# Optimization experiments

Hardware: AMD Instinct MI355X
Metric: run time of the kernel (lower is better)

## Reference

```python
import jax, jax.numpy as jnp
import numpy as np

B, Cin, Cout, H, W = 8, 256, 256, 56, 56
KH, KW, PAD = 3, 3, 1
K = KH * KW
EPS = 1e-5


def _conv3x3(x, w, b):
    # x: [B,Cin,H,W], w: [O,Cin,3,3] -> [B,O,H,W] (stride 1, pad 1)
    y = jax.lax.conv_general_dilated(x, w, window_strides=(1, 1),
                                     padding=((PAD, PAD), (PAD, PAD)),
                                     dimension_numbers=('NCHW', 'OIHW', 'NCHW'))
    return y + b[None, :, None, None]


def _bilinear_gather(x, py, px):
    # x: [B,Cin,H,W]; py/px: [B,K,H,W] fractional sample coords (zero padding)
    y0 = jnp.floor(py); x0 = jnp.floor(px)
    ly = py - y0; lx = px - x0
    y0i = y0.astype(jnp.int32); x0i = x0.astype(jnp.int32)
    y1i = y0i + 1; x1i = x0i + 1
    xf = x.reshape(B, Cin, H * W)

    def corner(yi, xi, wgt):
        valid = ((yi >= 0) & (yi < H) & (xi >= 0) & (xi < W)).astype(x.dtype)
        idx = (jnp.clip(yi, 0, H - 1) * W + jnp.clip(xi, 0, W - 1)).reshape(B, K * H * W)
        v = jax.vmap(lambda xb, ib: xb[:, ib])(xf, idx)  # [B,Cin,K*H*W]
        v = v.reshape(B, Cin, K, H, W)
        return v * (wgt * valid)[:, None]

    return (corner(y0i, x0i, (1 - ly) * (1 - lx)) +
            corner(y0i, x1i, (1 - ly) * lx) +
            corner(y1i, x0i, ly * (1 - lx)) +
            corner(y1i, x1i, ly * lx))


def setup_inputs():
    key = jax.random.key(0)
    ks = jax.random.split(key, 4)
    x = jax.random.normal(ks[0], (B, Cin, H, W), jnp.float32)
    w_off = jax.random.normal(ks[1], (2 * K, Cin, KH, KW), jnp.float32) * 0.01
    b_off = jnp.zeros((2 * K,), jnp.float32)
    w_conv = jax.random.normal(ks[2], (Cout, Cin, KH, KW), jnp.float32) * (1.0 / np.sqrt(Cin * K))
    gamma = jnp.ones((Cout,), jnp.float32)
    beta = jnp.zeros((Cout,), jnp.float32)
    run_mean = jnp.zeros((Cout,), jnp.float32)
    run_var = jnp.ones((Cout,), jnp.float32)
    return {"x": x, "w_off": w_off, "b_off": b_off, "w_conv": w_conv,
            "gamma": gamma, "beta": beta, "run_mean": run_mean, "run_var": run_var}


def reference(x, w_off, b_off, w_conv, gamma, beta, run_mean, run_var):
    # 1) learned offsets: [B, 2K, H, W] -> [B, K, 2(y,x), H, W]
    off = _conv3x3(x, w_off, b_off).reshape(B, K, 2, H, W)
    dy, dx = off[:, :, 0], off[:, :, 1]
    ky = jnp.repeat(jnp.arange(KH, dtype=x.dtype), KW)  # [K]
    kx = jnp.tile(jnp.arange(KW, dtype=x.dtype), KH)
    py = jnp.arange(H, dtype=x.dtype)[None, None, :, None] - PAD + ky[None, :, None, None] + dy
    px = jnp.arange(W, dtype=x.dtype)[None, None, None, :] - PAD + kx[None, :, None, None] + dx
    # 2) bilinear gather -> [B, Cin, K, H, W]; 3) conv reduction over (Cin, K)
    val = _bilinear_gather(x, py, px)
    out = jnp.einsum('bikhw,oik->bohw', val, w_conv.reshape(Cout, Cin, K))
    # 4) BatchNorm (eval: running stats) + ReLU
    inv = gamma / jnp.sqrt(run_var + EPS)
    bn = (out - run_mean[None, :, None, None]) * inv[None, :, None, None] + beta[None, :, None, None]
    return jnp.maximum(bn, 0.0)
```

## Files before the change

### kernel.cpp

```cpp
#include <hip/hip_runtime.h>


#define BATCH 8
#define CIN   256
#define COUT  256
#define HH    56
#define WW    56
#define HW    (HH*WW)
#define NPIX  (BATCH*HW)
#define KTAP  9
#define KG    (KTAP*CIN)
#define NKT   (KG/64)

typedef unsigned short ushortT;
typedef _Float16 f16x8 __attribute__((ext_vector_type(8)));
typedef float f32x4 __attribute__((ext_vector_type(4)));

__device__ __forceinline__ f16x8 lds_ldh8(const ushortT* p) {
    uint4 u = *(const uint4*)p;
    return __builtin_bit_cast(f16x8, u);
}
__device__ __forceinline__ unsigned packh2(float v0, float v1) {
    _Float16 h0 = (_Float16)v0, h1 = (_Float16)v1;
    return (unsigned)__builtin_bit_cast(unsigned short, h0)
         | ((unsigned)__builtin_bit_cast(unsigned short, h1) << 16);
}

__global__ __launch_bounds__(256) void k0_transpose(
    const float* __restrict__ x, float* __restrict__ xt)
{
    __shared__ float t[64][65];
    const int bid = blockIdx.x;
    const int b   = bid / 196;
    const int r   = bid % 196;
    const int hw0 = (r >> 2) * 64;
    const int c0  = (r & 3) * 64;
    const int tid = threadIdx.x;

    {
        const int c_l = tid >> 2, ch = (tid & 3) * 16;
        const float* src = x + ((size_t)(b*CIN + c0 + c_l))*HW + hw0 + ch;
        float4 v0 = *(const float4*)(src + 0);
        float4 v1 = *(const float4*)(src + 4);
        float4 v2 = *(const float4*)(src + 8);
        float4 v3 = *(const float4*)(src + 12);
        *(float4*)&t[c_l][ch + 0]  = v0;
        *(float4*)&t[c_l][ch + 4]  = v1;
        *(float4*)&t[c_l][ch + 8]  = v2;
        *(float4*)&t[c_l][ch + 12] = v3;
    }
    __syncthreads();
    {
        const int hw_l = tid >> 2, cc = (tid & 3) * 16;
        float* dst = xt + ((size_t)(b*HW + hw0 + hw_l))*CIN + c0 + cc;
        #pragma unroll
        for (int q = 0; q < 4; ++q) {
            float4 o;
            o.x = t[cc + q*4 + 0][hw_l];
            o.y = t[cc + q*4 + 1][hw_l];
            o.z = t[cc + q*4 + 2][hw_l];
            o.w = t[cc + q*4 + 3][hw_l];
            *(float4*)(dst + q*4) = o;
        }
    }
}

__global__ void k2a_prep_w(const float* __restrict__ wconv, const float* __restrict__ woff,
                           ushortT* __restrict__ Ah, ushortT* __restrict__ A0h)
{
    int id = blockIdx.x*256 + threadIdx.x;
    if (id < COUT*KG) {
        int m = id / KG, kg = id % KG;
        int k = kg >> 8, i = kg & 255;
        float f = wconv[(m*CIN + i)*9 + k];
        int kt = kg >> 6, kk = kg & 63;
        _Float16 h = (_Float16)f;
        Ah[kt*16384 + m*64 + (kk ^ ((m & 7) << 3))] = __builtin_bit_cast(unsigned short, h);
    } else if (id < COUT*KG + 32*KG) {
        int id2 = id - COUT*KG;
        int m = id2 / KG, kg = id2 % KG;
        int k = kg >> 8, i = kg & 255;
        float f = (m < 18) ? woff[(m*CIN + i)*9 + k] : 0.f;
        int kt = kg >> 6, kk = kg & 63;
        _Float16 h = (_Float16)f;
        A0h[kt*2048 + m*64 + (kk ^ ((m & 7) << 3))] = __builtin_bit_cast(unsigned short, h);
    }
}

__global__ __launch_bounds__(256) void k1_offmfma(
    const float* __restrict__ xt, const ushortT* __restrict__ A0h_g,
    const float* __restrict__ b_off, float* __restrict__ off)
{
    __shared__ __align__(16) ushortT A0[32*64];
    __shared__ __align__(16) ushortT Bh[64*64];

    const int tid = threadIdx.x;
    const int bn0 = blockIdx.x * 64;
    const int wv = tid >> 6, lane = tid & 63;
    const int l16 = lane & 15, lq = lane >> 4;
    const int px_l = tid >> 2, g2 = tid & 3;

    const int np = bn0 + px_l;
    const int hw = np % HW;
    const int h = hw / WW, w = hw % WW;

    f32x4 acc[2] = {};

    for (int kt = 0; kt < NKT; ++kt) {
        const int tap = kt >> 2, ic = kt & 3;
        const int ky = tap / 3 - 1, kx = tap % 3 - 1;
        __syncthreads();
        __builtin_amdgcn_global_load_lds(
            (const __attribute__((address_space(1))) unsigned*)((const char*)A0h_g + kt*4096 + tid*16),
            (__attribute__((address_space(3))) unsigned*)((char*)A0 + wv*1024), 16, 0, 0);
        {
            const int hs = h + ky, ws = w + kx;
            const bool valid = (hs >= 0 && hs < HH && ws >= 0 && ws < WW);
            const float* p = xt + ((size_t)(np + ky*WW + kx))*CIN + ic*64 + g2*16;
            float4 v0, v1, v2, v3;
            if (valid) {
                v0 = *(const float4*)(p + 0);  v1 = *(const float4*)(p + 4);
                v2 = *(const float4*)(p + 8);  v3 = *(const float4*)(p + 12);
            } else {
                v0 = v1 = v2 = v3 = make_float4(0.f, 0.f, 0.f, 0.f);
            }
            uint4 h0, h1;
            h0.x = packh2(v0.x, v0.y); h0.y = packh2(v0.z, v0.w);
            h0.z = packh2(v1.x, v1.y); h0.w = packh2(v1.z, v1.w);
            h1.x = packh2(v2.x, v2.y); h1.y = packh2(v2.z, v2.w);
            h1.z = packh2(v3.x, v3.y); h1.w = packh2(v3.z, v3.w);
            const int base = g2 * 16;
            *(uint4*)&Bh[px_l*64 + ((base + 0) ^ ((px_l & 7) << 3))] = h0;
            *(uint4*)&Bh[px_l*64 + ((base + 8) ^ ((px_l & 7) << 3))] = h1;
        }
        __syncthreads();
        #pragma unroll
        for (int ks = 0; ks < 2; ++ks) {
            const int kk0 = ks*32 + lq*8;
            f16x8 a0, a1, b;
            {
                const int m0 = l16, m1 = 16 + l16;
                a0 = lds_ldh8(&A0[m0*64 + (kk0 ^ ((m0 & 7) << 3))]);
                a1 = lds_ldh8(&A0[m1*64 + (kk0 ^ ((m1 & 7) << 3))]);
            }
            {
                const int n = wv*16 + l16;
                b = lds_ldh8(&Bh[n*64 + (kk0 ^ ((n & 7) << 3))]);
            }
            acc[0] = __builtin_amdgcn_mfma_f32_16x16x32_f16(a0, b, acc[0], 0, 0, 0);
            acc[1] = __builtin_amdgcn_mfma_f32_16x16x32_f16(a1, b, acc[1], 0, 0, 0);
        }
    }
    const int n = bn0 + wv*16 + l16;
    const int b2 = n / HW, hw2 = n % HW;
    #pragma unroll
    for (int mf = 0; mf < 2; ++mf) {
        #pragma unroll
        for (int r = 0; r < 4; ++r) {
            const int m = mf*16 + lq*4 + r;
            if (m < 18)
                off[((size_t)b2*18 + m)*HW + hw2] = acc[mf][r] + b_off[m];
        }
    }
}

__global__ void k2b_meta(const float* __restrict__ off,
                         int* __restrict__ midx, float* __restrict__ mw)
{
    int id = blockIdx.x*256 + threadIdx.x;
    if (id >= KTAP*NPIX) return;
    int k = id / NPIX, np = id % NPIX;
    int b = np / HW, hw = np % HW;
    int h = hw / WW, w = hw % WW;
    float dy = off[((size_t)b*18 + 2*k    )*HW + hw];
    float dx = off[((size_t)b*18 + 2*k + 1)*HW + hw];
    float py = (float)(h - 1 + (k / 3)) + dy;
    float px = (float)(w - 1 + (k % 3)) + dx;
    py = fminf(fmaxf(py, -10000.f), 10000.f);
    px = fminf(fmaxf(px, -10000.f), 10000.f);
    float y0f = floorf(py), x0f = floorf(px);
    int y0 = (int)y0f, x0 = (int)x0f;
    float ly = py - y0f, lx = px - x0f;
    #pragma unroll
    for (int c = 0; c < 4; ++c) {
        int yi = y0 + (c >> 1), xi = x0 + (c & 1);
        float wgt = ((c >> 1) ? ly : 1.f - ly) * ((c & 1) ? lx : 1.f - lx);
        bool valid = (yi >= 0 && yi < HH && xi >= 0 && xi < WW);
        int yc = min(max(yi, 0), HH-1), xc = min(max(xi, 0), WW-1);
        midx[(c*KTAP + k)*NPIX + np] = (b*HW + yc*WW + xc) * CIN;
        mw  [(c*KTAP + k)*NPIX + np] = valid ? wgt : 0.f;
    }
}

__global__ void k2c_bn(const float* __restrict__ g, const float* __restrict__ be,
                       const float* __restrict__ rm, const float* __restrict__ rv,
                       float* __restrict__ scale, float* __restrict__ shift)
{
    int t = threadIdx.x;
    float inv = g[t] / sqrtf(rv[t] + 1e-5f);
    scale[t] = inv;
    shift[t] = be[t] - rm[t]*inv;
}

__global__ __launch_bounds__(512) void k3_main(
    const float* __restrict__ xt, const int* __restrict__ midx, const float* __restrict__ mw,
    const ushortT* __restrict__ Ah_g, const float* __restrict__ scale_g,
    const float* __restrict__ shift_g, float* __restrict__ out)
{
    __shared__ __align__(16) ushortT Ah_t[256*64];
    __shared__ __align__(16) ushortT Bh_t[64*64];
    __shared__ __align__(16) ushortT Bl_t[64*64];
    __shared__ int   s_midx[256];
    __shared__ float s_mw[256];
    __shared__ float s_scale[256], s_shift[256];

    const int tid = threadIdx.x;
    const int bn0 = blockIdx.x * 64;
    if (tid < 256) { s_scale[tid] = scale_g[tid]; s_shift[tid] = shift_g[tid]; }

    const int wv = tid >> 6, lane = tid & 63;
    const int l16 = lane & 15, lq = lane >> 4;
    const int mbase = (wv >> 1) * 64;
    const int nbase = (wv & 1) * 32;
    const int px_l = tid >> 3, g = tid & 7;

    f32x4 acc[4][2] = {};

    for (int kt = 0; kt < NKT; ++kt) {
        const int tap = kt >> 2, ic = kt & 3;
        __syncthreads();
        if (ic == 0) {
            if (tid < 256) {
                const int c = tid >> 6, px = tid & 63;
                s_midx[tid] = midx[(c*KTAP + tap)*NPIX + bn0 + px];
                s_mw[tid]   = mw  [(c*KTAP + tap)*NPIX + bn0 + px];
            }
            __syncthreads();
        }
        {
            const char* gh = (const char*)Ah_g + (size_t)kt*32768;
            #pragma unroll
            for (int it = 0; it < 4; ++it) {
                __builtin_amdgcn_global_load_lds(
                    (const __attribute__((address_space(1))) unsigned*)(gh + it*8192 + tid*16),
                    (__attribute__((address_space(3))) unsigned*)((char*)Ah_t + it*8192 + wv*1024), 16, 0, 0);
            }
        }
        {
            const float* base = xt + (size_t)(ic*64 + g*8);
            const float* p0 = base + s_midx[0*64 + px_l]; const float fw0 = s_mw[0*64 + px_l];
            const float* p1 = base + s_midx[1*64 + px_l]; const float fw1 = s_mw[1*64 + px_l];
            const float* p2 = base + s_midx[2*64 + px_l]; const float fw2 = s_mw[2*64 + px_l];
            const float* p3 = base + s_midx[3*64 + px_l]; const float fw3 = s_mw[3*64 + px_l];
            float4 a0 = *(const float4*)(p0 + 0), a1 = *(const float4*)(p0 + 4);
            float4 b0 = *(const float4*)(p1 + 0), b1 = *(const float4*)(p1 + 4);
            float4 c0 = *(const float4*)(p2 + 0), c1 = *(const float4*)(p2 + 4);
            float4 d0 = *(const float4*)(p3 + 0), d1 = *(const float4*)(p3 + 4);
            float v[8];
            v[0] = fw0*a0.x + fw1*b0.x + fw2*c0.x + fw3*d0.x;
            v[1] = fw0*a0.y + fw1*b0.y + fw2*c0.y + fw3*d0.y;
            v[2] = fw0*a0.z + fw1*b0.z + fw2*c0.z + fw3*d0.z;
            v[3] = fw0*a0.w + fw1*b0.w + fw2*c0.w + fw3*d0.w;
            v[4] = fw0*a1.x + fw1*b1.x + fw2*c1.x + fw3*d1.x;
            v[5] = fw0*a1.y + fw1*b1.y + fw2*c1.y + fw3*d1.y;
            v[6] = fw0*a1.z + fw1*b1.z + fw2*c1.z + fw3*d1.z;
            v[7] = fw0*a1.w + fw1*b1.w + fw2*c1.w + fw3*d1.w;
            uint4 hi, lo;
            float r[8];
            #pragma unroll
            for (int j = 0; j < 8; ++j) {
                _Float16 hh = (_Float16)v[j];
                r[j] = v[j] - (float)hh;
            }
            hi.x = packh2(v[0], v[1]); hi.y = packh2(v[2], v[3]);
            hi.z = packh2(v[4], v[5]); hi.w = packh2(v[6], v[7]);
            lo.x = packh2(r[0], r[1]); lo.y = packh2(r[2], r[3]);
            lo.z = packh2(r[4], r[5]); lo.w = packh2(r[6], r[7]);
            const int idx = px_l*64 + ((g*8) ^ ((px_l & 7) << 3));
            *(uint4*)&Bh_t[idx] = hi;
            *(uint4*)&Bl_t[idx] = lo;
        }
        __syncthreads();
        #pragma unroll
        for (int ks = 0; ks < 2; ++ks) {
            const int kk0 = ks*32 + lq*8;
            f16x8 a[4], bh[2], bl[2];
            #pragma unroll
            for (int mf = 0; mf < 4; ++mf) {
                const int m = mbase + mf*16 + l16;
                a[mf] = lds_ldh8(&Ah_t[m*64 + (kk0 ^ ((m & 7) << 3))]);
            }
            #pragma unroll
            for (int nf = 0; nf < 2; ++nf) {
                const int n = nbase + nf*16 + l16;
                const int idx = n*64 + (kk0 ^ ((n & 7) << 3));
                bh[nf] = lds_ldh8(&Bh_t[idx]);
                bl[nf] = lds_ldh8(&Bl_t[idx]);
            }
            #pragma unroll
            for (int mf = 0; mf < 4; ++mf) {
                #pragma unroll
                for (int nf = 0; nf < 2; ++nf) {
                    acc[mf][nf] = __builtin_amdgcn_mfma_f32_16x16x32_f16(a[mf], bh[nf], acc[mf][nf], 0, 0, 0);
                    acc[mf][nf] = __builtin_amdgcn_mfma_f32_16x16x32_f16(a[mf], bl[nf], acc[mf][nf], 0, 0, 0);
                }
            }
        }
    }
    #pragma unroll
    for (int mf = 0; mf < 4; ++mf) {
        #pragma unroll
        for (int nf = 0; nf < 2; ++nf) {
            const int n = bn0 + nbase + nf*16 + l16;
            const int b = n / HW, hw = n % HW;
            const int m0 = mbase + mf*16 + lq*4;
            float* op = out + ((size_t)b*COUT + m0)*HW + hw;
            const f32x4 v = acc[mf][nf];
            #pragma unroll
            for (int r = 0; r < 4; ++r) {
                float val = fmaxf(v[r]*s_scale[m0 + r] + s_shift[m0 + r], 0.f);
                op[(size_t)r*HW] = val;
            }
        }
    }
}

extern "C" void kernel_launch(void* const* d_in, const int* in_sizes, int n_in,
                              void* d_out, int out_size, void* d_ws, size_t ws_size,
                              hipStream_t stream)
{
    const float* x      = (const float*)d_in[0];
    const float* w_off  = (const float*)d_in[1];
    const float* b_off  = (const float*)d_in[2];
    const float* w_conv = (const float*)d_in[3];
    const float* gamma  = (const float*)d_in[4];
    const float* beta   = (const float*)d_in[5];
    const float* rmean  = (const float*)d_in[6];
    const float* rvar   = (const float*)d_in[7];
    float* out = (float*)d_out;
    char* ws = (char*)d_ws;

    float*   xt    = (float*)(ws + 0);
    float*   off   = (float*)(ws + 25690112);
    int*     midx  = (int*)  (ws + 27496448);
    float*   mwt   = (float*)(ws + 31109120);
    ushortT* Ah    = (ushortT*)(ws + 34721792);
    ushortT* A0h   = (ushortT*)(ws + 35901440);
    float*   scale = (float*)(ws + 36048896);
    float*   shift = (float*)(ws + 36049920);

    hipLaunchKernelGGL(k0_transpose, dim3(1568), dim3(256), 0, stream, x, xt);
    hipLaunchKernelGGL(k2a_prep_w, dim3((COUT*KG + 32*KG + 255)/256), dim3(256), 0, stream,
                       w_conv, w_off, Ah, A0h);
    hipLaunchKernelGGL(k2c_bn, dim3(1), dim3(256), 0, stream, gamma, beta, rmean, rvar, scale, shift);
    hipLaunchKernelGGL(k1_offmfma, dim3(NPIX/64), dim3(256), 0, stream, xt, A0h, b_off, off);
    hipLaunchKernelGGL(k2b_meta, dim3((KTAP*NPIX + 255)/256), dim3(256), 0, stream, off, midx, mwt);
    hipLaunchKernelGGL(k3_main, dim3(NPIX/64), dim3(512), 0, stream,
                       xt, midx, mwt, Ah, scale, shift, out);
}
```

Before: 241.8 us.

## Software-pipeline deformable gather with MFMA, split-K offset conv, compact per-tap metadata

The main kernel now double-buffers the B tiles, so the next k-step's bilinear gather loads are issued before the current MFMA phase, with explicit waitcnt/barrier control and raised priority around the MFMAs. Bilinear metadata shrinks to one packed int4 per pixel-tap, and corner indices and weights are recomputed in-kernel instead of read as 8 arrays. The offset conv is split-K across four blocks per tile, accumulating with atomicAdd into a memset buffer, with the bias moved into the meta kernel. Blocks are remapped so consecutive block IDs span the eight batch images, and the BN prep kernel is folded into weight prep. The cost is atomics, extra register pressure, and fragile manual vmcnt accounting.

```diff
diff --git a/kernel.cpp b/kernel.cpp
--- a/kernel.cpp
+++ b/kernel.cpp
@@ -6,11 +6,11 @@
 #define COUT  256
 #define HH    56
 #define WW    56
-#define HW    (HH*WW)
-#define NPIX  (BATCH*HW)
+#define HW    3136
+#define NPIX  25088
 #define KTAP  9
-#define KG    (KTAP*CIN)
-#define NKT   (KG/64)
+#define KG    2304
+#define NKT   36
 
 typedef unsigned short ushortT;
 typedef _Float16 f16x8 __attribute__((ext_vector_type(8)));
@@ -30,7 +30,7 @@
     const float* __restrict__ x, float* __restrict__ xt)
 {
     __shared__ float t[64][65];
-    const int bid = blockIdx.x;
+    const int bid = (blockIdx.x & 7) * 196 + (blockIdx.x >> 3);
     const int b   = bid / 196;
     const int r   = bid % 196;
     const int hw0 = (r >> 2) * 64;
@@ -65,8 +65,11 @@
     }
 }
 
-__global__ void k2a_prep_w(const float* __restrict__ wconv, const float* __restrict__ woff,
-                           ushortT* __restrict__ Ah, ushortT* __restrict__ A0h)
+__global__ void k2a_prep(const float* __restrict__ wconv, const float* __restrict__ woff,
+                         const float* __restrict__ g, const float* __restrict__ be,
+                         const float* __restrict__ rm, const float* __restrict__ rv,
+                         ushortT* __restrict__ Ah, ushortT* __restrict__ A0h,
+                         float* __restrict__ scale, float* __restrict__ shift)
 {
     int id = blockIdx.x*256 + threadIdx.x;
     if (id < COUT*KG) {
@@ -84,38 +87,49 @@
         int kt = kg >> 6, kk = kg & 63;
         _Float16 h = (_Float16)f;
         A0h[kt*2048 + m*64 + (kk ^ ((m & 7) << 3))] = __builtin_bit_cast(unsigned short, h);
+    } else if (id < COUT*KG + 32*KG + 256) {
+        int t = id - (COUT*KG + 32*KG);
+        float inv = g[t] / sqrtf(rv[t] + 1e-5f);
+        scale[t] = inv;
+        shift[t] = be[t] - rm[t]*inv;
     }
 }
 
 __global__ __launch_bounds__(256) void k1_offmfma(
     const float* __restrict__ xt, const ushortT* __restrict__ A0h_g,
-    const float* __restrict__ b_off, float* __restrict__ off)
+    float* __restrict__ off)
 {
     __shared__ __align__(16) ushortT A0[32*64];
     __shared__ __align__(16) ushortT Bh[64*64];
 
     const int tid = threadIdx.x;
-    const int bn0 = blockIdx.x * 64;
+    const int x8 = blockIdx.x & 7;
+    const int j  = blockIdx.x >> 3;
+    const int tile = x8*49 + (j % 49);
+    const int ks = j / 49;
+    const int bn0 = tile * 64;
+
     const int wv = tid >> 6, lane = tid & 63;
     const int l16 = lane & 15, lq = lane >> 4;
     const int px_l = tid >> 2, g2 = tid & 3;
 
     const int np = bn0 + px_l;
-    const int hw = np % HW;
+    const int hw = np - x8*HW;
     const int h = hw / WW, w = hw % WW;
 
     f32x4 acc[2] = {};
 
-    for (int kt = 0; kt < NKT; ++kt) {
-        const int tap = kt >> 2, ic = kt & 3;
+    for (int t = 0; t < 9; ++t) {
+        const int ktg = ks*9 + t;
+        const int tap = ktg >> 2, ic = ktg & 3;
         const int ky = tap / 3 - 1, kx = tap % 3 - 1;
         __syncthreads();
         __builtin_amdgcn_global_load_lds(
-            (const __attribute__((address_space(1))) unsigned*)((const char*)A0h_g + kt*4096 + tid*16),
+            (const __attribute__((address_space(1))) unsigned*)((const char*)A0h_g + ktg*4096 + tid*16),
             (__attribute__((address_space(3))) unsigned*)((char*)A0 + wv*1024), 16, 0, 0);
         {
-            const int hs = h + ky, ws = w + kx;
-            const bool valid = (hs >= 0 && hs < HH && ws >= 0 && ws < WW);
+            const int hs = h + ky, ws2 = w + kx;
+            const bool valid = (hs >= 0 && hs < HH && ws2 >= 0 && ws2 < WW);
             const float* p = xt + ((size_t)(np + ky*WW + kx))*CIN + ic*64 + g2*16;
             float4 v0, v1, v2, v3;
             if (valid) {
@@ -135,9 +149,9 @@
         }
         __syncthreads();
         #pragma unroll
-        for (int ks = 0; ks < 2; ++ks) {
-            const int kk0 = ks*32 + lq*8;
-            f16x8 a0, a1, b;
+        for (int kss = 0; kss < 2; ++kss) {
+            const int kk0 = kss*32 + lq*8;
+            f16x8 a0, a1, bfr;
             {
                 const int m0 = l16, m1 = 16 + l16;
                 a0 = lds_ldh8(&A0[m0*64 + (kk0 ^ ((m0 & 7) << 3))]);
@@ -145,77 +159,65 @@
             }
             {
                 const int n = wv*16 + l16;
-                b = lds_ldh8(&Bh[n*64 + (kk0 ^ ((n & 7) << 3))]);
+                bfr = lds_ldh8(&Bh[n*64 + (kk0 ^ ((n & 7) << 3))]);
             }
-            acc[0] = __builtin_amdgcn_mfma_f32_16x16x32_f16(a0, b, acc[0], 0, 0, 0);
-            acc[1] = __builtin_amdgcn_mfma_f32_16x16x32_f16(a1, b, acc[1], 0, 0, 0);
+            acc[0] = __builtin_amdgcn_mfma_f32_16x16x32_f16(a0, bfr, acc[0], 0, 0, 0);
+            acc[1] = __builtin_amdgcn_mfma_f32_16x16x32_f16(a1, bfr, acc[1], 0, 0, 0);
         }
     }
     const int n = bn0 + wv*16 + l16;
-    const int b2 = n / HW, hw2 = n % HW;
+    const int hw2 = n - x8*HW;
     #pragma unroll
     for (int mf = 0; mf < 2; ++mf) {
         #pragma unroll
         for (int r = 0; r < 4; ++r) {
             const int m = mf*16 + lq*4 + r;
             if (m < 18)
-                off[((size_t)b2*18 + m)*HW + hw2] = acc[mf][r] + b_off[m];
-        }
-    }
-}
-
-__global__ void k2b_meta(const float* __restrict__ off,
-                         int* __restrict__ midx, float* __restrict__ mw)
+                atomicAdd(&off[((size_t)x8*18 + m)*HW + hw2], acc[mf][r]);
+        }
+    }
+}
+
+__global__ void k2b_meta(const float* __restrict__ off, const float* __restrict__ b_off,
+                         int* __restrict__ meta)
 {
     int id = blockIdx.x*256 + threadIdx.x;
     if (id >= KTAP*NPIX) return;
     int k = id / NPIX, np = id % NPIX;
     int b = np / HW, hw = np % HW;
     int h = hw / WW, w = hw % WW;
-    float dy = off[((size_t)b*18 + 2*k    )*HW + hw];
-    float dx = off[((size_t)b*18 + 2*k + 1)*HW + hw];
+    float dy = off[((size_t)b*18 + 2*k    )*HW + hw] + b_off[2*k];
+    float dx = off[((size_t)b*18 + 2*k + 1)*HW + hw] + b_off[2*k + 1];
     float py = (float)(h - 1 + (k / 3)) + dy;
     float px = (float)(w - 1 + (k % 3)) + dx;
-    py = fminf(fmaxf(py, -10000.f), 10000.f);
-    px = fminf(fmaxf(px, -10000.f), 10000.f);
+    py = fminf(fmaxf(py, -30000.f), 30000.f);
+    px = fminf(fmaxf(px, -30000.f), 30000.f);
     float y0f = floorf(py), x0f = floorf(px);
     int y0 = (int)y0f, x0 = (int)x0f;
     float ly = py - y0f, lx = px - x0f;
-    #pragma unroll
-    for (int c = 0; c < 4; ++c) {
-        int yi = y0 + (c >> 1), xi = x0 + (c & 1);
-        float wgt = ((c >> 1) ? ly : 1.f - ly) * ((c & 1) ? lx : 1.f - lx);
-        bool valid = (yi >= 0 && yi < HH && xi >= 0 && xi < WW);
-        int yc = min(max(yi, 0), HH-1), xc = min(max(xi, 0), WW-1);
-        midx[(c*KTAP + k)*NPIX + np] = (b*HW + yc*WW + xc) * CIN;
-        mw  [(c*KTAP + k)*NPIX + np] = valid ? wgt : 0.f;
-    }
-}
-
-__global__ void k2c_bn(const float* __restrict__ g, const float* __restrict__ be,
-                       const float* __restrict__ rm, const float* __restrict__ rv,
-                       float* __restrict__ scale, float* __restrict__ shift)
-{
-    int t = threadIdx.x;
-    float inv = g[t] / sqrtf(rv[t] + 1e-5f);
-    scale[t] = inv;
-    shift[t] = be[t] - rm[t]*inv;
-}
-
-__global__ __launch_bounds__(512) void k3_main(
-    const float* __restrict__ xt, const int* __restrict__ midx, const float* __restrict__ mw,
+    int4 m;
+    m.x = (y0 & 0xFFFF) | ((x0 & 0xFFFF) << 16);
+    m.y = __float_as_int(ly);
+    m.z = __float_as_int(lx);
+    m.w = 0;
+    *(int4*)&meta[(k*NPIX + np)*4] = m;
+}
+
+__global__ __launch_bounds__(512, 4) void k3_main(
+    const float* __restrict__ xt, const int* __restrict__ meta,
     const ushortT* __restrict__ Ah_g, const float* __restrict__ scale_g,
     const float* __restrict__ shift_g, float* __restrict__ out)
 {
     __shared__ __align__(16) ushortT Ah_t[256*64];
-    __shared__ __align__(16) ushortT Bh_t[64*64];
-    __shared__ __align__(16) ushortT Bl_t[64*64];
-    __shared__ int   s_midx[256];
-    __shared__ float s_mw[256];
+    __shared__ __align__(16) ushortT Bh_t[2][64*64];
+    __shared__ __align__(16) ushortT Bl_t[2][64*64];
     __shared__ float s_scale[256], s_shift[256];
 
     const int tid = threadIdx.x;
-    const int bn0 = blockIdx.x * 64;
+    const int bimg = blockIdx.x & 7;
+    const int lt   = blockIdx.x >> 3;
+    const int tile = bimg*49 + lt;
+    const int bn0  = tile * 64;
     if (tid < 256) { s_scale[tid] = scale_g[tid]; s_shift[tid] = shift_g[tid]; }
 
     const int wv = tid >> 6, lane = tid & 63;
@@ -223,98 +225,139 @@
     const int mbase = (wv >> 1) * 64;
     const int nbase = (wv & 1) * 32;
     const int px_l = tid >> 3, g = tid & 7;
-
+    const int np = bn0 + px_l;
+
+    int   mi[4];
+    float mwv[4];
+    f32x4 Gc[4][2];
     f32x4 acc[4][2] = {};
 
+    #define LOAD_META(tap_) do {                                               \
+        int4 m_ = *(const int4*)&meta[((tap_)*NPIX + np)*4];                   \
+        int y0_ = (short)(m_.x & 0xFFFF);                                      \
+        int x0_ = (short)(((unsigned)m_.x) >> 16);                             \
+        float ly_ = __int_as_float(m_.y), lx_ = __int_as_float(m_.z);          \
+        float wy0_ = 1.f - ly_, wx0_ = 1.f - lx_;                              \
+        _Pragma("unroll")                                                      \
+        for (int c_ = 0; c_ < 4; ++c_) {                                       \
+            int yi_ = y0_ + (c_ >> 1), xi_ = x0_ + (c_ & 1);                   \
+            bool v_ = (yi_ >= 0) && (yi_ < HH) && (xi_ >= 0) && (xi_ < WW);    \
+            int yc_ = min(max(yi_, 0), HH-1), xc_ = min(max(xi_, 0), WW-1);    \
+            mi[c_] = (bimg*HW + yc_*WW + xc_)*CIN;                             \
+            float wy_ = (c_ >> 1) ? ly_ : wy0_;                                \
+            float wx_ = (c_ & 1) ? lx_ : wx0_;                                 \
+            mwv[c_] = v_ ? wy_*wx_ : 0.f;                                      \
+        }                                                                      \
+    } while (0)
+
+    #define ISSUE_GATHER(j_) do {                                              \
+        const float* base_ = xt + ((j_) & 3)*64 + g*8;                         \
+        _Pragma("unroll")                                                      \
+        for (int c_ = 0; c_ < 4; ++c_) {                                       \
+            const float* p_ = base_ + mi[c_];                                  \
+            Gc[c_][0] = *(const f32x4*)p_;                                     \
+            Gc[c_][1] = *(const f32x4*)(p_ + 4);                               \
+        }                                                                      \
+    } while (0)
+
+    #define BLEND_WRITE(nxt_) do {                                             \
+        float v_[8];                                                           \
+        _Pragma("unroll")                                                      \
+        for (int q_ = 0; q_ < 4; ++q_) {                                       \
+            v_[q_]   = mwv[0]*Gc[0][0][q_] + mwv[1]*Gc[1][0][q_]               \
+                     + mwv[2]*Gc[2][0][q_] + mwv[3]*Gc[3][0][q_];              \
+            v_[4+q_] = mwv[0]*Gc[0][1][q_] + mwv[1]*Gc[1][1][q_]               \
+                     + mwv[2]*Gc[2][1][q_] + mwv[3]*Gc[3][1][q_];              \
+        }                                                                      \
+        uint4 hi_, lo_;                                                        \
+        float r_[8];                                                           \
+        _Pragma("unroll")                                                      \
+        for (int q_ = 0; q_ < 8; ++q_) {                                       \
+            _Float16 hh_ = (_Float16)v_[q_];                                   \
+            r_[q_] = v_[q_] - (float)hh_;                                      \
+        }                                                                      \
+        hi_.x = packh2(v_[0], v_[1]); hi_.y = packh2(v_[2], v_[3]);            \
+        hi_.z = packh2(v_[4], v_[5]); hi_.w = packh2(v_[6], v_[7]);            \
+        lo_.x = packh2(r_[0], r_[1]); lo_.y = packh2(r_[2], r_[3]);            \
+        lo_.z = packh2(r_[4], r_[5]); lo_.w = packh2(r_[6], r_[7]);            \
+        const int idx_ = px_l*64 + ((g*8) ^ ((px_l & 7) << 3));                \
+        *(uint4*)&Bh_t[nxt_][idx_] = hi_;                                      \
+        *(uint4*)&Bl_t[nxt_][idx_] = lo_;                                      \
+    } while (0)
+
+    #define ISSUE_A(j_) do {                                                   \
+        const char* gs_ = (const char*)Ah_g + (size_t)(j_)*32768;              \
+        _Pragma("unroll")                                                      \
+        for (int it_ = 0; it_ < 4; ++it_)                                      \
+            __builtin_amdgcn_global_load_lds(                                  \
+                (const __attribute__((address_space(1))) unsigned*)(gs_ + it_*8192 + tid*16), \
+                (__attribute__((address_space(3))) unsigned*)((char*)Ah_t + it_*8192 + wv*1024), \
+                16, 0, 0);                                                     \
+    } while (0)
+
+    #define MFMA_PHASE(cur_) do {                                              \
+        __builtin_amdgcn_s_setprio(1);                                         \
+        _Pragma("unroll")                                                      \
+        for (int ks_ = 0; ks_ < 2; ++ks_) {                                    \
+            const int kk0_ = ks_*32 + lq*8;                                    \
+            f16x8 a_[4], bh_[2], bl_[2];                                       \
+            _Pragma("unroll")                                                  \
+            for (int mf_ = 0; mf_ < 4; ++mf_) {                                \
+                const int m_ = mbase + mf_*16 + l16;                           \
+                a_[mf_] = lds_ldh8(&Ah_t[m_*64 + (kk0_ ^ ((m_ & 7) << 3))]);   \
+            }                                                                  \
+            _Pragma("unroll")                                                  \
+            for (int nf_ = 0; nf_ < 2; ++nf_) {                                \
+                const int n_ = nbase + nf_*16 + l16;                           \
+                const int ix_ = n_*64 + (kk0_ ^ ((n_ & 7) << 3));              \
+                bh_[nf_] = lds_ldh8(&Bh_t[cur_][ix_]);                         \
+                bl_[nf_] = lds_ldh8(&Bl_t[cur_][ix_]);                         \
+            }                                                                  \
+            _Pragma("unroll")                                                  \
+            for (int mf_ = 0; mf_ < 4; ++mf_) {                                \
+                _Pragma("unroll")                                              \
+                for (int nf_ = 0; nf_ < 2; ++nf_) {                            \
+                    acc[mf_][nf_] = __builtin_amdgcn_mfma_f32_16x16x32_f16(a_[mf_], bh_[nf_], acc[mf_][nf_], 0, 0, 0); \
+                    acc[mf_][nf_] = __builtin_amdgcn_mfma_f32_16x16x32_f16(a_[mf_], bl_[nf_], acc[mf_][nf_], 0, 0, 0); \
+                }                                                              \
+            }                                                                  \
+        }                                                                      \
+        __builtin_amdgcn_s_setprio(0);                                         \
+    } while (0)
+
+    LOAD_META(0);
+    ISSUE_GATHER(0);
+    ISSUE_A(0);
+    BLEND_WRITE(0);
+    asm volatile("s_waitcnt lgkmcnt(0)" ::: "memory");
+    __builtin_amdgcn_s_barrier();
+
     for (int kt = 0; kt < NKT; ++kt) {
-        const int tap = kt >> 2, ic = kt & 3;
-        __syncthreads();
-        if (ic == 0) {
-            if (tid < 256) {
-                const int c = tid >> 6, px = tid & 63;
-                s_midx[tid] = midx[(c*KTAP + tap)*NPIX + bn0 + px];
-                s_mw[tid]   = mw  [(c*KTAP + tap)*NPIX + bn0 + px];
-            }
-            __syncthreads();
-        }
-        {
-            const char* gh = (const char*)Ah_g + (size_t)kt*32768;
-            #pragma unroll
-            for (int it = 0; it < 4; ++it) {
-                __builtin_amdgcn_global_load_lds(
-                    (const __attribute__((address_space(1))) unsigned*)(gh + it*8192 + tid*16),
-                    (__attribute__((address_space(3))) unsigned*)((char*)Ah_t + it*8192 + wv*1024), 16, 0, 0);
-            }
-        }
-        {
-            const float* base = xt + (size_t)(ic*64 + g*8);
-            const float* p0 = base + s_midx[0*64 + px_l]; const float fw0 = s_mw[0*64 + px_l];
-            const float* p1 = base + s_midx[1*64 + px_l]; const float fw1 = s_mw[1*64 + px_l];
-            const float* p2 = base + s_midx[2*64 + px_l]; const float fw2 = s_mw[2*64 + px_l];
-            const float* p3 = base + s_midx[3*64 + px_l]; const float fw3 = s_mw[3*64 + px_l];
-            float4 a0 = *(const float4*)(p0 + 0), a1 = *(const float4*)(p0 + 4);
-            float4 b0 = *(const float4*)(p1 + 0), b1 = *(const float4*)(p1 + 4);
-            float4 c0 = *(const float4*)(p2 + 0), c1 = *(const float4*)(p2 + 4);
-            float4 d0 = *(const float4*)(p3 + 0), d1 = *(const float4*)(p3 + 4);
-            float v[8];
-            v[0] = fw0*a0.x + fw1*b0.x + fw2*c0.x + fw3*d0.x;
-            v[1] = fw0*a0.y + fw1*b0.y + fw2*c0.y + fw3*d0.y;
-            v[2] = fw0*a0.z + fw1*b0.z + fw2*c0.z + fw3*d0.z;
-            v[3] = fw0*a0.w + fw1*b0.w + fw2*c0.w + fw3*d0.w;
-            v[4] = fw0*a1.x + fw1*b1.x + fw2*c1.x + fw3*d1.x;
-            v[5] = fw0*a1.y + fw1*b1.y + fw2*c1.y + fw3*d1.y;
-            v[6] = fw0*a1.z + fw1*b1.z + fw2*c1.z + fw3*d1.z;
-            v[7] = fw0*a1.w + fw1*b1.w + fw2*c1.w + fw3*d1.w;
-            uint4 hi, lo;
-            float r[8];
-            #pragma unroll
-            for (int j = 0; j < 8; ++j) {
-                _Float16 hh = (_Float16)v[j];
-                r[j] = v[j] - (float)hh;
-            }
-            hi.x = packh2(v[0], v[1]); hi.y = packh2(v[2], v[3]);
-            hi.z = packh2(v[4], v[5]); hi.w = packh2(v[6], v[7]);
-            lo.x = packh2(r[0], r[1]); lo.y = packh2(r[2], r[3]);
-            lo.z = packh2(r[4], r[5]); lo.w = packh2(r[6], r[7]);
-            const int idx = px_l*64 + ((g*8) ^ ((px_l & 7) << 3));
-            *(uint4*)&Bh_t[idx] = hi;
-            *(uint4*)&Bl_t[idx] = lo;
-        }
-        __syncthreads();
-        #pragma unroll
-        for (int ks = 0; ks < 2; ++ks) {
-            const int kk0 = ks*32 + lq*8;
-            f16x8 a[4], bh[2], bl[2];
-            #pragma unroll
-            for (int mf = 0; mf < 4; ++mf) {
-                const int m = mbase + mf*16 + l16;
-                a[mf] = lds_ldh8(&Ah_t[m*64 + (kk0 ^ ((m & 7) << 3))]);
-            }
-            #pragma unroll
-            for (int nf = 0; nf < 2; ++nf) {
-                const int n = nbase + nf*16 + l16;
-                const int idx = n*64 + (kk0 ^ ((n & 7) << 3));
-                bh[nf] = lds_ldh8(&Bh_t[idx]);
-                bl[nf] = lds_ldh8(&Bl_t[idx]);
-            }
-            #pragma unroll
-            for (int mf = 0; mf < 4; ++mf) {
-                #pragma unroll
-                for (int nf = 0; nf < 2; ++nf) {
-                    acc[mf][nf] = __builtin_amdgcn_mfma_f32_16x16x32_f16(a[mf], bh[nf], acc[mf][nf], 0, 0, 0);
-                    acc[mf][nf] = __builtin_amdgcn_mfma_f32_16x16x32_f16(a[mf], bl[nf], acc[mf][nf], 0, 0, 0);
-                }
-            }
-        }
-    }
+        const int cur = kt & 1;
+        if (kt + 1 < NKT) {
+            if (((kt + 1) & 3) == 0) LOAD_META((kt + 1) >> 2);
+            ISSUE_GATHER(kt + 1);
+            asm volatile("s_waitcnt vmcnt(8)" ::: "memory");
+        } else {
+            asm volatile("s_waitcnt vmcnt(0)" ::: "memory");
+        }
+        __builtin_amdgcn_s_barrier();
+        __builtin_amdgcn_sched_barrier(0);
+        MFMA_PHASE(cur);
+        if (kt + 1 < NKT) BLEND_WRITE(cur ^ 1);
+        asm volatile("s_waitcnt lgkmcnt(0)" ::: "memory");
+        __builtin_amdgcn_s_barrier();
+        if (kt + 1 < NKT) ISSUE_A(kt + 1);
+    }
+
+    const int hwb = lt * 64;
     #pragma unroll
     for (int mf = 0; mf < 4; ++mf) {
         #pragma unroll
         for (int nf = 0; nf < 2; ++nf) {
-            const int n = bn0 + nbase + nf*16 + l16;
-            const int b = n / HW, hw = n % HW;
+            const int hwloc = hwb + nbase + nf*16 + l16;
             const int m0 = mbase + mf*16 + lq*4;
-            float* op = out + ((size_t)b*COUT + m0)*HW + hw;
+            float* op = out + ((size_t)bimg*COUT + m0)*HW + hwloc;
             const f32x4 v = acc[mf][nf];
             #pragma unroll
             for (int r = 0; r < 4; ++r) {
@@ -323,6 +366,11 @@
             }
         }
     }
+    #undef LOAD_META
+    #undef ISSUE_GATHER
+    #undef BLEND_WRITE
+    #undef ISSUE_A
+    #undef MFMA_PHASE
 }
 
 extern "C" void kernel_launch(void* const* d_in, const int* in_sizes, int n_in,
@@ -342,19 +390,19 @@
 
     float*   xt    = (float*)(ws + 0);
     float*   off   = (float*)(ws + 25690112);
-    int*     midx  = (int*)  (ws + 27496448);
-    float*   mwt   = (float*)(ws + 31109120);
-    ushortT* Ah    = (ushortT*)(ws + 34721792);
-    ushortT* A0h   = (ushortT*)(ws + 35901440);
-    float*   scale = (float*)(ws + 36048896);
-    float*   shift = (float*)(ws + 36049920);
-
+    int*     meta  = (int*)  (ws + 27496448);
+    ushortT* Ah    = (ushortT*)(ws + 31109120);
+    ushortT* A0h   = (ushortT*)(ws + 32288768);
+    float*   scale = (float*)(ws + 32436224);
+    float*   shift = (float*)(ws + 32437248);
+
+    hipMemsetAsync(off, 0, 1806336, stream);
     hipLaunchKernelGGL(k0_transpose, dim3(1568), dim3(256), 0, stream, x, xt);
-    hipLaunchKernelGGL(k2a_prep_w, dim3((COUT*KG + 32*KG + 255)/256), dim3(256), 0, stream,
-                       w_conv, w_off, Ah, A0h);
-    hipLaunchKernelGGL(k2c_bn, dim3(1), dim3(256), 0, stream, gamma, beta, rmean, rvar, scale, shift);
-    hipLaunchKernelGGL(k1_offmfma, dim3(NPIX/64), dim3(256), 0, stream, xt, A0h, b_off, off);
-    hipLaunchKernelGGL(k2b_meta, dim3((KTAP*NPIX + 255)/256), dim3(256), 0, stream, off, midx, mwt);
-    hipLaunchKernelGGL(k3_main, dim3(NPIX/64), dim3(512), 0, stream,
-                       xt, midx, mwt, Ah, scale, shift, out);
-}
+    hipLaunchKernelGGL(k2a_prep, dim3((COUT*KG + 32*KG + 256 + 255)/256), dim3(256), 0, stream,
+                       w_conv, w_off, gamma, beta, rmean, rvar, Ah, A0h, scale, shift);
+    hipLaunchKernelGGL(k1_offmfma, dim3(1568), dim3(256), 0, stream, xt, A0h, off);
+    hipLaunchKernelGGL(k2b_meta, dim3((KTAP*NPIX + 255)/256), dim3(256), 0, stream,
+                       off, b_off, meta);
+    hipLaunchKernelGGL(k3_main, dim3(392), dim3(512), 0, stream,
+                       xt, meta, Ah, scale, shift, out);
+}
```

Measured after the change: 216.6 us. 1.12x faster.
